# Performance work log

Measured on AMD Instinct MI355X. Metric: run time of the kernel, lower is better.

## Reference

```python
import jax, jax.numpy as jnp
import numpy as np
from jax import lax

S, B, T = 512, 1024, 64


def setup_inputs() -> dict:
    key = jax.random.key(0)
    k_em, k_tags, k_len, k_st, k_en, k_tr = jax.random.split(key, 6)
    emissions = jax.random.normal(k_em, (S, B, T), dtype=jnp.float32)
    tags = jax.random.randint(k_tags, (S, B), 0, T, dtype=jnp.int32)
    lengths = jax.random.randint(k_len, (B,), 1, S + 1, dtype=jnp.int32)  # mask[0] all on
    start_transitions = jax.random.uniform(k_st, (T,), jnp.float32, -0.1, 0.1)
    end_transitions = jax.random.uniform(k_en, (T,), jnp.float32, -0.1, 0.1)
    transitions = jax.random.uniform(k_tr, (T, T), jnp.float32, -0.1, 0.1)
    return {"emissions": emissions, "tags": tags, "lengths": lengths,
            "start_transitions": start_transitions,
            "end_transitions": end_transitions,
            "transitions": transitions}


def reference(emissions, tags, lengths, start_transitions, end_transitions, transitions):
    # emissions: [S,B,T], tags: [S,B], lengths: [B]. reduction='sum'.
    s, b, t = emissions.shape
    mask = jnp.arange(s)[:, None] < lengths[None, :]          # [S,B] bool, mask[0] all True
    maskf = mask.astype(emissions.dtype)
    batch_idx = jnp.arange(b)

    # ---- numerator: score of the gold tag path (vectorized over time) ----
    score = start_transitions[tags[0]] + emissions[0, batch_idx, tags[0]]  # [B]
    trans_scores = transitions[tags[:-1], tags[1:]]                        # [S-1,B]
    emit_scores = jnp.take_along_axis(emissions, tags[..., None].astype(jnp.int32), axis=2)[..., 0]  # [S,B]
    score = score + jnp.sum((trans_scores + emit_scores[1:]) * maskf[1:], axis=0)
    last_tags = tags[lengths - 1, batch_idx]
    score = score + end_transitions[last_tags]

    # ---- denominator: log-partition via forward-algorithm scan ----
    init = start_transitions + emissions[0]                    # [B,T]
    def step(carry, inp):
        em, m = inp                                            # em: [B,T], m: [B]
        nxt = jax.nn.logsumexp(carry[:, :, None] + transitions[None, :, :] + em[:, None, :], axis=1)
        carry = jnp.where(m[:, None], nxt, carry)
        return carry, None
    final, _ = lax.scan(step, init, (emissions[1:], mask[1:]))
    denom = jax.nn.logsumexp(final + end_transitions, axis=1)  # [B]

    llh = score - denom
    return llh.sum()
```

## Files before the change

kernel.cpp:

```cpp
#include <hip/hip_runtime.h>

#define SEQ 512
#define BATCH 1024
#define NT 64
#define BT (BATCH * NT)
#define NUMER_BLOCKS 512
#define LN2F 0.69314718055994531f

__global__ __launch_bounds__(64, 1) void crf_fused(
    const float* __restrict__ em, const int* __restrict__ tags,
    const int* __restrict__ lens, const float* __restrict__ st,
    const float* __restrict__ en, const float* __restrict__ tr,
    float* __restrict__ out)
{
    __shared__ __align__(16) float p_sh[NT];
    const int lane = threadIdx.x;

    if (blockIdx.x < BATCH) {
        const int b = blockIdx.x;
        const int L = lens[b];

        float e[NT];
        #pragma unroll
        for (int i = 0; i < NT; ++i) e[i] = __expf(tr[i * NT + lane]);

        const float* emb = em + (size_t)b * NT + lane;

        float x0 = st[lane] + emb[0];
        float xs = __uint_as_float(__builtin_amdgcn_readfirstlane(__float_as_uint(x0)));
        float p = __expf(x0 - xs);
        int ksum = 0;

        float em_n0 = 0.f, em_n1 = 0.f;
        if (L > 1) em_n0 = emb[(size_t)1 * BT];
        if (L > 2) em_n1 = emb[(size_t)2 * BT];

        for (int s = 1; s < L; ++s) {
            p_sh[lane] = p;
            float eexp = __expf(em_n0);
            em_n0 = em_n1;
            if (s + 2 < L) em_n1 = emb[(size_t)(s + 2) * BT];
            asm volatile("s_waitcnt lgkmcnt(0)" ::: "memory");

            float d0 = 0.f, d1 = 0.f, d2 = 0.f, d3 = 0.f;
            float d4 = 0.f, d5 = 0.f, d6 = 0.f, d7 = 0.f;
            const float4* pv = reinterpret_cast<const float4*>(p_sh);
            #pragma unroll
            for (int i = 0; i < NT; i += 8) {
                float4 a = pv[i / 4];
                float4 c = pv[i / 4 + 1];
                d0 = fmaf(a.x, e[i + 0], d0);
                d1 = fmaf(a.y, e[i + 1], d1);
                d2 = fmaf(a.z, e[i + 2], d2);
                d3 = fmaf(a.w, e[i + 3], d3);
                d4 = fmaf(c.x, e[i + 4], d4);
                d5 = fmaf(c.y, e[i + 5], d5);
                d6 = fmaf(c.z, e[i + 6], d6);
                d7 = fmaf(c.w, e[i + 7], d7);
            }
            float dot = ((d0 + d1) + (d2 + d3)) + ((d4 + d5) + (d6 + d7));
            float pj = dot * eexp;

            unsigned b0 = __builtin_amdgcn_readfirstlane(__float_as_uint(pj));
            int k = (int)(b0 >> 23) - 127;
            ksum += k;
            float scale = __uint_as_float((unsigned)(127 - k) << 23);
            p = pj * scale;
        }

        float term = p * __expf(en[lane]);
        #pragma unroll
        for (int d = 32; d > 0; d >>= 1) term += __shfl_xor(term, d);
        if (lane == 0)
            atomicAdd(out, -(xs + (float)ksum * LN2F + __logf(term)));
    } else {
        const int t0 = (blockIdx.x - BATCH) * 64 + lane;
        float acc = 0.f;
        for (int idx = t0; idx < SEQ * BATCH; idx += NUMER_BLOCKS * 64) {
            int b = idx & (BATCH - 1);
            int s = idx >> 10;
            int L = lens[b];
            int tg = tags[s * BATCH + b];
            float v = 0.f;
            if (s == 0) {
                v = st[tg] + em[(size_t)b * NT + tg];
            } else if (s < L) {
                int tp = tags[(s - 1) * BATCH + b];
                v = tr[tp * NT + tg] + em[(size_t)s * BT + (size_t)b * NT + tg];
            }
            if (s == L - 1) v += en[tg];
            acc += v;
        }
        #pragma unroll
        for (int d = 32; d > 0; d >>= 1) acc += __shfl_xor(acc, d);
        if (lane == 0) atomicAdd(out, acc);
    }
}

extern "C" void kernel_launch(void* const* d_in, const int* in_sizes, int n_in,
                              void* d_out, int out_size, void* d_ws, size_t ws_size,
                              hipStream_t stream)
{
    const float* emissions = (const float*)d_in[0];
    const int*   tags      = (const int*)d_in[1];
    const int*   lengths   = (const int*)d_in[2];
    const float* start_tr  = (const float*)d_in[3];
    const float* end_tr    = (const float*)d_in[4];
    const float* trans     = (const float*)d_in[5];
    float* out = (float*)d_out;

    hipMemsetAsync(out, 0, sizeof(float), stream);

    crf_fused<<<BATCH + NUMER_BLOCKS, 64, 0, stream>>>(
        emissions, tags, lengths, start_tr, end_tr, trans, out);
}
```

Baseline: 185.8 us.

## Batch 16 sequences per wave and run CRF forward recursion on bf16 MFMA

Replaces the one-sequence-per-block scalar FMA dot product with a 16-sequence-per-wave recursion that uses bf16 MFMA 16x16x32 to multiply exp(transitions) by the probability vectors. Emissions are staged into LDS with async global_load_lds double buffering in chunks of 4 timesteps, and the MFMA output is transposed back into B-operand layout through LDS. Per-sequence power-of-two rescaling is deferred by one step. The blocks drop from 1024 to 64, which shortens the serial per-step latency but lowers parallelism. Rounding the probabilities to bf16 adds precision risk.

```diff
diff --git a/kernel.cpp b/kernel.cpp
--- a/kernel.cpp
+++ b/kernel.cpp
@@ -4,8 +4,26 @@
 #define BATCH 1024
 #define NT 64
 #define BT (BATCH * NT)
+#define GC 16
+#define NGROUP (BATCH / GC)
+#define CHUNK 4
 #define NUMER_BLOCKS 512
 #define LN2F 0.69314718055994531f
+
+typedef __attribute__((ext_vector_type(8))) short short8;
+typedef __attribute__((ext_vector_type(4))) float f32x4;
+typedef __attribute__((ext_vector_type(4))) unsigned u32x4;
+
+__device__ __forceinline__ unsigned cvt_pk_bf16(float lo, float hi) {
+    unsigned r;
+    asm("v_cvt_pk_bf16_f32 %0, %1, %2" : "=v"(r) : "v"(lo), "v"(hi));
+    return r;
+}
+
+__device__ __forceinline__ short8 mk8(const unsigned* u) {
+    u32x4 t = {u[0], u[1], u[2], u[3]};
+    return __builtin_bit_cast(short8, t);
+}
 
 __global__ __launch_bounds__(64, 1) void crf_fused(
     const float* __restrict__ em, const int* __restrict__ tags,
@@ -13,68 +31,140 @@
     const float* __restrict__ en, const float* __restrict__ tr,
     float* __restrict__ out)
 {
-    __shared__ __align__(16) float p_sh[NT];
+    __shared__ __align__(16) float em_lds[2][CHUNK][GC][NT];
+    __shared__ unsigned y_lds[32 * 17];
     const int lane = threadIdx.x;
-
-    if (blockIdx.x < BATCH) {
-        const int b = blockIdx.x;
-        const int L = lens[b];
-
-        float e[NT];
-        #pragma unroll
-        for (int i = 0; i < NT; ++i) e[i] = __expf(tr[i * NT + lane]);
-
-        const float* emb = em + (size_t)b * NT + lane;
-
-        float x0 = st[lane] + emb[0];
-        float xs = __uint_as_float(__builtin_amdgcn_readfirstlane(__float_as_uint(x0)));
-        float p = __expf(x0 - xs);
-        int ksum = 0;
-
-        float em_n0 = 0.f, em_n1 = 0.f;
-        if (L > 1) em_n0 = emb[(size_t)1 * BT];
-        if (L > 2) em_n1 = emb[(size_t)2 * BT];
-
-        for (int s = 1; s < L; ++s) {
-            p_sh[lane] = p;
-            float eexp = __expf(em_n0);
-            em_n0 = em_n1;
-            if (s + 2 < L) em_n1 = emb[(size_t)(s + 2) * BT];
-            asm volatile("s_waitcnt lgkmcnt(0)" ::: "memory");
-
-            float d0 = 0.f, d1 = 0.f, d2 = 0.f, d3 = 0.f;
-            float d4 = 0.f, d5 = 0.f, d6 = 0.f, d7 = 0.f;
-            const float4* pv = reinterpret_cast<const float4*>(p_sh);
-            #pragma unroll
-            for (int i = 0; i < NT; i += 8) {
-                float4 a = pv[i / 4];
-                float4 c = pv[i / 4 + 1];
-                d0 = fmaf(a.x, e[i + 0], d0);
-                d1 = fmaf(a.y, e[i + 1], d1);
-                d2 = fmaf(a.z, e[i + 2], d2);
-                d3 = fmaf(a.w, e[i + 3], d3);
-                d4 = fmaf(c.x, e[i + 4], d4);
-                d5 = fmaf(c.y, e[i + 5], d5);
-                d6 = fmaf(c.z, e[i + 6], d6);
-                d7 = fmaf(c.w, e[i + 7], d7);
-            }
-            float dot = ((d0 + d1) + (d2 + d3)) + ((d4 + d5) + (d6 + d7));
-            float pj = dot * eexp;
-
-            unsigned b0 = __builtin_amdgcn_readfirstlane(__float_as_uint(pj));
-            int k = (int)(b0 >> 23) - 127;
-            ksum += k;
-            float scale = __uint_as_float((unsigned)(127 - k) << 23);
-            p = pj * scale;
+    const int c  = lane & 15;
+    const int hi = lane >> 4;
+
+    if (blockIdx.x < NGROUP) {
+        const int cb = blockIdx.x * GC;
+        const int Lc = lens[cb + c];
+        int maxL = Lc;
+        #pragma unroll
+        for (int d = 1; d < 16; d <<= 1) maxL = max(maxL, __shfl_xor(maxL, d));
+
+        unsigned Au[4][2][4];
+        #pragma unroll
+        for (int t = 0; t < 4; ++t)
+            #pragma unroll
+            for (int f = 0; f < 2; ++f)
+                #pragma unroll
+                for (int j2 = 0; j2 < 4; ++j2) {
+                    int k = 32 * f + 8 * hi + 2 * j2;
+                    int m = 16 * t + c;
+                    Au[t][f][j2] = cvt_pk_bf16(__expf(tr[k * NT + m]),
+                                               __expf(tr[(k + 1) * NT + m]));
+                }
+        short8 A8[4][2];
+        #pragma unroll
+        for (int t = 0; t < 4; ++t) {
+            A8[t][0] = mk8(Au[t][0]);
+            A8[t][1] = mk8(Au[t][1]);
         }
 
-        float term = p * __expf(en[lane]);
-        #pragma unroll
-        for (int d = 32; d > 0; d >>= 1) term += __shfl_xor(term, d);
-        if (lane == 0)
-            atomicAdd(out, -(xs + (float)ksum * LN2F + __logf(term)));
+        const float xs = st[0] + em[(size_t)(cb + c) * NT];
+        unsigned Bu[2][4];
+        #pragma unroll
+        for (int f = 0; f < 2; ++f)
+            #pragma unroll
+            for (int j2 = 0; j2 < 4; ++j2) {
+                int k = 32 * f + 8 * hi + 2 * j2;
+                float p0 = __expf(st[k]     + em[(size_t)(cb + c) * NT + k]     - xs);
+                float p1 = __expf(st[k + 1] + em[(size_t)(cb + c) * NT + k + 1] - xs);
+                Bu[f][j2] = cvt_pk_bf16(p0, p1);
+            }
+
+        auto stage = [&](int ch) {
+            const int sb = ch * CHUNK;
+            #pragma unroll
+            for (int i = 0; i < CHUNK; ++i)
+                #pragma unroll
+                for (int q = 0; q < 4; ++q) {
+                    const float* g = em + (size_t)(sb + i) * BT + cb * NT
+                                     + q * 256 + lane * 4;
+                    __builtin_amdgcn_global_load_lds(
+                        (const __attribute__((address_space(1))) void*)g,
+                        (__attribute__((address_space(3))) void*)
+                            (&em_lds[ch & 1][i][0][0] + q * 256),
+                        16, 0, 0);
+                }
+        };
+        const int nch = (maxL + CHUNK - 1) / CHUNK;
+        stage(0);
+        asm volatile("s_waitcnt vmcnt(0)" ::: "memory");
+        if (nch > 1) stage(1);
+
+        int ksum = 0, pend_k = 0;
+        float pend_scale = 1.0f;
+        const f32x4 zacc = {0.f, 0.f, 0.f, 0.f};
+
+        for (int s = 1; s < maxL; ++s) {
+            const int ch = s >> 2;
+            if ((s & 3) == 0) {
+                asm volatile("s_waitcnt vmcnt(0)" ::: "memory");
+                if (ch + 1 < nch) stage(ch + 1);
+            }
+
+            short8 B0 = mk8(Bu[0]), B1 = mk8(Bu[1]);
+            f32x4 acc[4];
+            #pragma unroll
+            for (int t = 0; t < 4; ++t) {
+                acc[t] = __builtin_amdgcn_mfma_f32_16x16x32_bf16(
+                    A8[t][0], B0, zacc, 0, 0, 0);
+                acc[t] = __builtin_amdgcn_mfma_f32_16x16x32_bf16(
+                    A8[t][1], B1, acc[t], 0, 0, 0);
+            }
+
+            const float4* erow = reinterpret_cast<const float4*>(
+                &em_lds[ch & 1][s & 3][c][0]);
+            #pragma unroll
+            for (int t = 0; t < 4; ++t) {
+                float4 e4 = erow[4 * t + hi];
+                float y0 = fminf(acc[t][0] * __expf(e4.x) * pend_scale, 1e30f);
+                float y1 = fminf(acc[t][1] * __expf(e4.y) * pend_scale, 1e30f);
+                float y2 = fminf(acc[t][2] * __expf(e4.z) * pend_scale, 1e30f);
+                float y3 = fminf(acc[t][3] * __expf(e4.w) * pend_scale, 1e30f);
+                y_lds[(8 * t + 2 * hi)     * 17 + c] = cvt_pk_bf16(y0, y1);
+                y_lds[(8 * t + 2 * hi + 1) * 17 + c] = cvt_pk_bf16(y2, y3);
+            }
+
+            unsigned u00 = y_lds[c];
+
+            const bool live = (s < Lc);
+            if (live) ksum += pend_k;
+
+            #pragma unroll
+            for (int f = 0; f < 2; ++f)
+                #pragma unroll
+                for (int j2 = 0; j2 < 4; ++j2) {
+                    unsigned v = y_lds[(16 * f + 4 * hi + j2) * 17 + c];
+                    Bu[f][j2] = live ? v : Bu[f][j2];
+                }
+
+            int kk = (int)((u00 >> 7) & 255) - 127;
+            kk = kk < -126 ? -126 : (kk > 126 ? 126 : kk);
+            pend_k = kk;
+            pend_scale = __uint_as_float((unsigned)(127 - kk) << 23);
+        }
+
+        float part = 0.f;
+        #pragma unroll
+        for (int f = 0; f < 2; ++f)
+            #pragma unroll
+            for (int j2 = 0; j2 < 4; ++j2) {
+                unsigned u = Bu[f][j2];
+                int k0 = 32 * f + 8 * hi + 2 * j2;
+                part += __uint_as_float(u << 16)          * __expf(en[k0]);
+                part += __uint_as_float(u & 0xffff0000u)  * __expf(en[k0 + 1]);
+            }
+        part += __shfl_xor(part, 16);
+        part += __shfl_xor(part, 32);
+        part = fmaxf(part, 1e-35f);
+        if (lane < 16)
+            atomicAdd(out, -(xs + (float)ksum * LN2F + __logf(part)));
     } else {
-        const int t0 = (blockIdx.x - BATCH) * 64 + lane;
+        const int t0 = (blockIdx.x - NGROUP) * 64 + lane;
         float acc = 0.f;
         for (int idx = t0; idx < SEQ * BATCH; idx += NUMER_BLOCKS * 64) {
             int b = idx & (BATCH - 1);
@@ -111,6 +201,6 @@
 
     hipMemsetAsync(out, 0, sizeof(float), stream);
 
-    crf_fused<<<BATCH + NUMER_BLOCKS, 64, 0, stream>>>(
+    crf_fused<<<NGROUP + NUMER_BLOCKS, 64, 0, stream>>>(
         emissions, tags, lengths, start_tr, end_tr, trans, out);
 }
```

Measured after the change: 367.7 us. 97.9% more time.
